# Optimization experiments

Measured on AMD Instinct MI355X. Metric: run time of the kernel, lower is better.

Reference implementation:

```python
import jax, jax.numpy as jnp
import numpy as np

N, C, HW = 32, 256, 64          # batch, in_channels, input_size
K = 128                          # n_clusters
S = 8                            # blocks per side
BLOCK = (HW + S - 1) // S        # = 8, padding_size = 0


def setup_inputs() -> dict:
    key = jax.random.key(0)
    k1, k2 = jax.random.split(key)
    x = jax.random.normal(k1, (N, C, HW, HW), dtype=jnp.float32)
    cluster_centers = jax.random.normal(k2, (K, C), dtype=jnp.float32)
    return {"x": x, "cluster_centers": cluster_centers}


def reference(x, cluster_centers):
    # --- Codebook: argmin over squared distances, computed without the
    x2 = jnp.sum(x * x, axis=1)                       # (N, H, W)
    c2 = jnp.sum(cluster_centers * cluster_centers, axis=1)  # (K,)
    xc = jnp.einsum('nchw,kc->nkhw', x, cluster_centers)     # (N, K, H, W)
    dist = x2[:, None] - 2.0 * xc + c2[None, :, None, None]
    code = jnp.argmin(dist, axis=1)                   # (N, H, W) int

    # --- BlockWiseHistogramEncoder: unfold into S*S non-overlapping
    # BLOCKxBLOCK blocks (padding_size == 0 here), one_hot(code+1), mean ---
    shifted = code + 1                                # values in [1, K]
    n = shifted.shape[0]
    blocks = shifted.reshape(n, S, BLOCK, S, BLOCK)
    blocks = blocks.transpose(0, 1, 3, 2, 4).reshape(n, S * S, BLOCK * BLOCK)
    onehot = (blocks[..., None] == jnp.arange(K + 1)).astype(jnp.float32)
    return onehot.mean(axis=2)                        # (N, S*S, K+1)
```

## Files before the change

### kernel.cpp

```cpp
#include <hip/hip_runtime.h>

#define C_DIM 256
#define K_DIM 128
#define HW_DIM 64
#define PIX 4096
#define N_IMG 32

using short8 = __attribute__((ext_vector_type(8))) short;
using f32x4  = __attribute__((ext_vector_type(4))) float;

__device__ __forceinline__ void lds_barrier() {
    asm volatile("s_waitcnt lgkmcnt(0)\n\ts_barrier" ::: "memory");
}

__device__ __forceinline__ unsigned long long umin64(unsigned long long a, unsigned long long b) {
    return a < b ? a : b;
}
__device__ __forceinline__ unsigned mono(float d) {
    unsigned u = __float_as_uint(d);
    return u ^ ((u & 0x80000000u) ? 0xFFFFFFFFu : 0x80000000u);
}

__device__ __forceinline__ void split3t(float v, unsigned& hu, unsigned& mu, unsigned& lu) {
    unsigned u = __float_as_uint(v);
    unsigned hf = u & 0xffff0000u;
    float r1 = v - __uint_as_float(hf);
    unsigned r1u = __float_as_uint(r1);
    unsigned mf = r1u & 0xffff0000u;
    float r2 = r1 - __uint_as_float(mf);
    hu = u; mu = r1u; lu = __float_as_uint(r2);
}

__global__ __launch_bounds__(64) void prep_kernel(const float* __restrict__ cl,
                                                  unsigned short* __restrict__ Bt,
                                                  float* __restrict__ c2) {
    int k = blockIdx.x;
    int lane = threadIdx.x;
    const float4* row = (const float4*)(cl + k * C_DIM);
    float4 v = row[lane];
    float vv[4] = {v.x, v.y, v.z, v.w};
    unsigned short* bk = Bt + k * 768 + lane * 4;
#pragma unroll
    for (int i = 0; i < 4; ++i) {
        unsigned hu, mu, lu;
        split3t(vv[i], hu, mu, lu);
        bk[i]       = (unsigned short)(hu >> 16);
        bk[256 + i] = (unsigned short)(mu >> 16);
        bk[512 + i] = (unsigned short)(lu >> 16);
    }
    if (lane == 0) {
        float s = 0.f;
#pragma unroll
        for (int i = 0; i < C_DIM / 4; ++i) {
            float4 u = row[i];
            s = fmaf(u.x, u.x, s);
            s = fmaf(u.y, u.y, s);
            s = fmaf(u.z, u.z, s);
            s = fmaf(u.w, u.w, s);
        }
        c2[k] = s;
    }
}

__global__ __launch_bounds__(256) void main_kernel(
    const float* __restrict__ x, const unsigned short* __restrict__ Bt,
    const float* __restrict__ c2v, unsigned char* __restrict__ code) {

    __shared__ __align__(16) unsigned short Ap[3 * 4096];
    __shared__ float x2p[2][128];
    unsigned long long* red = (unsigned long long*)Ap;

    const int t    = threadIdx.x;
    const int lane = t & 63;
    const int w    = t >> 6;
    const int q    = lane >> 4;
    const int l15  = lane & 15;

    const int px = t & 127;
    const int h  = t >> 7;

    const int b   = blockIdx.x;
    const int img = b >> 5;
    const int pb  = (b & 31) * 128;

    const float* xg = x + (size_t)img * (C_DIM * PIX) + pb + px;

    f32x4 acc[8][2];
#pragma unroll
    for (int m = 0; m < 8; ++m)
#pragma unroll
        for (int ns = 0; ns < 2; ++ns) acc[m][ns] = (f32x4){0.f, 0.f, 0.f, 0.f};

    float xr[16];
#pragma unroll
    for (int j = 0; j < 16; ++j) xr[j] = xg[(size_t)(h * 16 + j) * PIX];

    float x2part = 0.f;
    const unsigned short* btb = Bt + (w * 32 + l15) * 768 + q * 8;

    const int wbase = (px >> 4) * 512 + (px & 15) * 8 + h * 2 * 128;

#pragma unroll 1
    for (int ci = 0; ci < 8; ++ci) {
        short8 bv[3][2];
#pragma unroll
        for (int p = 0; p < 3; ++p) {
            bv[p][0] = *(const short8*)(btb + p * 256 + ci * 32);
            bv[p][1] = *(const short8*)(btb + 16 * 768 + p * 256 + ci * 32);
        }

#pragma unroll
        for (int g = 0; g < 2; ++g) {
            unsigned p0[4], p1[4], p2[4];
#pragma unroll
            for (int jj = 0; jj < 4; ++jj) {
                float v0 = xr[g * 8 + jj * 2], v1 = xr[g * 8 + jj * 2 + 1];
                unsigned h0, m0, l0, h1, m1, l1;
                split3t(v0, h0, m0, l0);
                split3t(v1, h1, m1, l1);
                p0[jj] = (h0 >> 16) | (h1 & 0xffff0000u);
                p1[jj] = (m0 >> 16) | (m1 & 0xffff0000u);
                p2[jj] = (l0 >> 16) | (l1 & 0xffff0000u);
                x2part = fmaf(v0, v0, x2part);
                x2part = fmaf(v1, v1, x2part);
            }
            int base = wbase + g * 128;
            *(uint4*)&Ap[base]            = make_uint4(p0[0], p0[1], p0[2], p0[3]);
            *(uint4*)&Ap[4096 + base]     = make_uint4(p1[0], p1[1], p1[2], p1[3]);
            *(uint4*)&Ap[8192 + base]     = make_uint4(p2[0], p2[1], p2[2], p2[3]);
        }
        if (ci == 7) x2p[h][px] = x2part;

        if (ci < 7) {
#pragma unroll
            for (int j = 0; j < 16; ++j)
                xr[j] = xg[(size_t)((ci + 1) * 32 + h * 16 + j) * PIX];
        }

        lds_barrier();

#pragma unroll
        for (int pa = 0; pa < 3; ++pa) {
#pragma unroll
            for (int mg = 0; mg < 4; ++mg) {
                const int m0 = mg * 2, m1 = mg * 2 + 1;
                short8 af0 = *(const short8*)&Ap[pa * 4096 + m0 * 512 + lane * 8];
                short8 af1 = *(const short8*)&Ap[pa * 4096 + m1 * 512 + lane * 8];
#pragma unroll
                for (int pb2 = 0; pb2 < 3; ++pb2) {
                    if (pb2 < 3 - pa) {
                        acc[m0][0] = __builtin_amdgcn_mfma_f32_16x16x32_bf16(af0, bv[pb2][0], acc[m0][0], 0, 0, 0);
                        acc[m0][1] = __builtin_amdgcn_mfma_f32_16x16x32_bf16(af0, bv[pb2][1], acc[m0][1], 0, 0, 0);
                        acc[m1][0] = __builtin_amdgcn_mfma_f32_16x16x32_bf16(af1, bv[pb2][0], acc[m1][0], 0, 0, 0);
                        acc[m1][1] = __builtin_amdgcn_mfma_f32_16x16x32_bf16(af1, bv[pb2][1], acc[m1][1], 0, 0, 0);
                    }
                }
            }
        }
        lds_barrier();
    }

    const float c2a0 = c2v[w * 32 + l15];
    const float c2a1 = c2v[w * 32 + 16 + l15];
    const unsigned n0 = (unsigned)(w * 32 + l15);
    const unsigned n1 = n0 + 16;

#pragma unroll
    for (int m = 0; m < 8; ++m) {
#pragma unroll
        for (int r = 0; r < 4; ++r) {
            int pxl = m * 16 + q * 4 + r;
            float x2v = x2p[0][pxl] + x2p[1][pxl];
            float d0 = (x2v - 2.0f * acc[m][0][r]) + c2a0;
            float d1 = (x2v - 2.0f * acc[m][1][r]) + c2a1;
            unsigned long long k0 = ((unsigned long long)mono(d0) << 32) | n0;
            unsigned long long k1 = ((unsigned long long)mono(d1) << 32) | n1;
            unsigned long long best = umin64(k0, k1);
            best = umin64(best, __shfl_xor(best, 1));
            best = umin64(best, __shfl_xor(best, 2));
            best = umin64(best, __shfl_xor(best, 4));
            best = umin64(best, __shfl_xor(best, 8));
            if (l15 == 0) red[w * 128 + pxl] = best;
        }
    }
    lds_barrier();

    if (t < 128) {
        unsigned long long m0 = umin64(umin64(red[t], red[128 + t]),
                                       umin64(red[256 + t], red[384 + t]));
        code[(size_t)img * PIX + pb + t] = (unsigned char)(m0 & 0xFFu);
    }
}

__global__ __launch_bounds__(256) void hist_kernel(const unsigned char* __restrict__ code,
                                                   float* __restrict__ out) {
    __shared__ int hist[4][K_DIM + 1];
    int wid = threadIdx.x >> 6, lane = threadIdx.x & 63;
    int b = blockIdx.x * 4 + wid;
    int n = b >> 6, sy = (b >> 3) & 7, sx = b & 7;

    hist[wid][lane] = 0;
    hist[wid][lane + 64] = 0;
    if (lane == 0) hist[wid][128] = 0;
    __syncthreads();

    int hh = sy * 8 + (lane >> 3);
    int ww = sx * 8 + (lane & 7);
    int c = code[n * PIX + hh * HW_DIM + ww];
    atomicAdd(&hist[wid][c + 1], 1);
    __syncthreads();

    const float inv = 1.0f / 64.0f;
    out[(size_t)b * (K_DIM + 1) + lane] = hist[wid][lane] * inv;
    out[(size_t)b * (K_DIM + 1) + 64 + lane] = hist[wid][lane + 64] * inv;
    if (lane == 0) out[(size_t)b * (K_DIM + 1) + 128] = hist[wid][128] * inv;
}

extern "C" void kernel_launch(void* const* d_in, const int* in_sizes, int n_in,
                              void* d_out, int out_size, void* d_ws, size_t ws_size,
                              hipStream_t stream) {
    const float* x  = (const float*)d_in[0];
    const float* cl = (const float*)d_in[1];
    float* out = (float*)d_out;

    unsigned short* Bt = (unsigned short*)d_ws;
    float* c2 = (float*)((char*)d_ws + 196608);
    unsigned char* code = (unsigned char*)d_ws + 197120;

    prep_kernel<<<K_DIM, 64, 0, stream>>>(cl, Bt, c2);
    main_kernel<<<(N_IMG * PIX) / 128, 256, 0, stream>>>(x, Bt, c2, code);
    hist_kernel<<<(N_IMG * 64) / 4, 256, 0, stream>>>(code, out);
}
```

Before: 226.3 us.

## Fuse histogram into main kernel and build MFMA operands in registers without LDS

Each block now handles one 64-pixel image row, and the four waves split the work two ways by pixel half and two ways by cluster half. The x operand fragments are split into bf16 pieces directly in registers instead of being staged through LDS, which removes the per-iteration barriers. The histogram kernel and the code buffer are gone: the main kernel adds 1/64 straight into the output with float atomics after a memset. In exchange each wave reloads more B fragments from global memory, and contention on the output atomics may add cost.

```diff
diff --git a/kernel.cpp b/kernel.cpp
--- a/kernel.cpp
+++ b/kernel.cpp
@@ -9,10 +9,6 @@
 using short8 = __attribute__((ext_vector_type(8))) short;
 using f32x4  = __attribute__((ext_vector_type(4))) float;
 
-__device__ __forceinline__ void lds_barrier() {
-    asm volatile("s_waitcnt lgkmcnt(0)\n\ts_barrier" ::: "memory");
-}
-
 __device__ __forceinline__ unsigned long long umin64(unsigned long long a, unsigned long long b) {
     return a < b ? a : b;
 }
@@ -23,11 +19,9 @@
 
 __device__ __forceinline__ void split3t(float v, unsigned& hu, unsigned& mu, unsigned& lu) {
     unsigned u = __float_as_uint(v);
-    unsigned hf = u & 0xffff0000u;
-    float r1 = v - __uint_as_float(hf);
+    float r1 = v - __uint_as_float(u & 0xffff0000u);
     unsigned r1u = __float_as_uint(r1);
-    unsigned mf = r1u & 0xffff0000u;
-    float r2 = r1 - __uint_as_float(mf);
+    float r2 = r1 - __uint_as_float(r1u & 0xffff0000u);
     hu = u; mu = r1u; lu = __float_as_uint(r2);
 }
 
@@ -62,158 +56,156 @@
     }
 }
 
-__global__ __launch_bounds__(256) void main_kernel(
+__global__ __launch_bounds__(256, 4) void main_kernel(
     const float* __restrict__ x, const unsigned short* __restrict__ Bt,
-    const float* __restrict__ c2v, unsigned char* __restrict__ code) {
-
-    __shared__ __align__(16) unsigned short Ap[3 * 4096];
-    __shared__ float x2p[2][128];
-    unsigned long long* red = (unsigned long long*)Ap;
+    const float* __restrict__ c2v, float* __restrict__ out) {
+
+    __shared__ unsigned long long red[2][64];
 
     const int t    = threadIdx.x;
     const int lane = t & 63;
     const int w    = t >> 6;
+    const int pg   = w >> 1;
+    const int kj   = w & 1;
     const int q    = lane >> 4;
     const int l15  = lane & 15;
 
-    const int px = t & 127;
-    const int h  = t >> 7;
-
     const int b   = blockIdx.x;
-    const int img = b >> 5;
-    const int pb  = (b & 31) * 128;
-
-    const float* xg = x + (size_t)img * (C_DIM * PIX) + pb + px;
-
-    f32x4 acc[8][2];
-#pragma unroll
-    for (int m = 0; m < 8; ++m)
-#pragma unroll
-        for (int ns = 0; ns < 2; ++ns) acc[m][ns] = (f32x4){0.f, 0.f, 0.f, 0.f};
-
-    float xr[16];
-#pragma unroll
-    for (int j = 0; j < 16; ++j) xr[j] = xg[(size_t)(h * 16 + j) * PIX];
-
-    float x2part = 0.f;
-    const unsigned short* btb = Bt + (w * 32 + l15) * 768 + q * 8;
-
-    const int wbase = (px >> 4) * 512 + (px & 15) * 8 + h * 2 * 128;
+    const int img = b >> 6;
+    const int row = b & 63;
+
+    const float* xg = x + (size_t)img * (C_DIM * PIX) + row * HW_DIM + pg * 32 + l15;
+
+    const unsigned short* bq0 = Bt + (size_t)(kj * 64 +  0 + l15) * 768 + q * 8;
+    const unsigned short* bq1 = Bt + (size_t)(kj * 64 + 16 + l15) * 768 + q * 8;
+    const unsigned short* bq2 = Bt + (size_t)(kj * 64 + 32 + l15) * 768 + q * 8;
+    const unsigned short* bq3 = Bt + (size_t)(kj * 64 + 48 + l15) * 768 + q * 8;
+
+    f32x4 acc[2][4];
+#pragma unroll
+    for (int mt = 0; mt < 2; ++mt)
+#pragma unroll
+        for (int nt = 0; nt < 4; ++nt) acc[mt][nt] = (f32x4){0.f, 0.f, 0.f, 0.f};
+
+    float x2m[2] = {0.f, 0.f};
+
+    float xv[2][8];
+#pragma unroll
+    for (int mt = 0; mt < 2; ++mt)
+#pragma unroll
+        for (int j = 0; j < 8; ++j)
+            xv[mt][j] = xg[(size_t)(q * 8 + j) * PIX + mt * 16];
 
 #pragma unroll 1
     for (int ci = 0; ci < 8; ++ci) {
-        short8 bv[3][2];
-#pragma unroll
-        for (int p = 0; p < 3; ++p) {
-            bv[p][0] = *(const short8*)(btb + p * 256 + ci * 32);
-            bv[p][1] = *(const short8*)(btb + 16 * 768 + p * 256 + ci * 32);
-        }
-
-#pragma unroll
-        for (int g = 0; g < 2; ++g) {
-            unsigned p0[4], p1[4], p2[4];
+        union U { unsigned u[4]; short8 s; };
+        short8 af[3][2];
+#pragma unroll
+        for (int mt = 0; mt < 2; ++mt) {
+            U ah, am, al;
 #pragma unroll
             for (int jj = 0; jj < 4; ++jj) {
-                float v0 = xr[g * 8 + jj * 2], v1 = xr[g * 8 + jj * 2 + 1];
+                float v0 = xv[mt][2 * jj], v1 = xv[mt][2 * jj + 1];
                 unsigned h0, m0, l0, h1, m1, l1;
                 split3t(v0, h0, m0, l0);
                 split3t(v1, h1, m1, l1);
-                p0[jj] = (h0 >> 16) | (h1 & 0xffff0000u);
-                p1[jj] = (m0 >> 16) | (m1 & 0xffff0000u);
-                p2[jj] = (l0 >> 16) | (l1 & 0xffff0000u);
-                x2part = fmaf(v0, v0, x2part);
-                x2part = fmaf(v1, v1, x2part);
-            }
-            int base = wbase + g * 128;
-            *(uint4*)&Ap[base]            = make_uint4(p0[0], p0[1], p0[2], p0[3]);
-            *(uint4*)&Ap[4096 + base]     = make_uint4(p1[0], p1[1], p1[2], p1[3]);
-            *(uint4*)&Ap[8192 + base]     = make_uint4(p2[0], p2[1], p2[2], p2[3]);
-        }
-        if (ci == 7) x2p[h][px] = x2part;
+                ah.u[jj] = (h0 >> 16) | (h1 & 0xffff0000u);
+                am.u[jj] = (m0 >> 16) | (m1 & 0xffff0000u);
+                al.u[jj] = (l0 >> 16) | (l1 & 0xffff0000u);
+                x2m[mt] = fmaf(v0, v0, x2m[mt]);
+                x2m[mt] = fmaf(v1, v1, x2m[mt]);
+            }
+            af[0][mt] = ah.s; af[1][mt] = am.s; af[2][mt] = al.s;
+        }
 
         if (ci < 7) {
 #pragma unroll
-            for (int j = 0; j < 16; ++j)
-                xr[j] = xg[(size_t)((ci + 1) * 32 + h * 16 + j) * PIX];
-        }
-
-        lds_barrier();
-
-#pragma unroll
-        for (int pa = 0; pa < 3; ++pa) {
-#pragma unroll
-            for (int mg = 0; mg < 4; ++mg) {
-                const int m0 = mg * 2, m1 = mg * 2 + 1;
-                short8 af0 = *(const short8*)&Ap[pa * 4096 + m0 * 512 + lane * 8];
-                short8 af1 = *(const short8*)&Ap[pa * 4096 + m1 * 512 + lane * 8];
-#pragma unroll
-                for (int pb2 = 0; pb2 < 3; ++pb2) {
-                    if (pb2 < 3 - pa) {
-                        acc[m0][0] = __builtin_amdgcn_mfma_f32_16x16x32_bf16(af0, bv[pb2][0], acc[m0][0], 0, 0, 0);
-                        acc[m0][1] = __builtin_amdgcn_mfma_f32_16x16x32_bf16(af0, bv[pb2][1], acc[m0][1], 0, 0, 0);
-                        acc[m1][0] = __builtin_amdgcn_mfma_f32_16x16x32_bf16(af1, bv[pb2][0], acc[m1][0], 0, 0, 0);
-                        acc[m1][1] = __builtin_amdgcn_mfma_f32_16x16x32_bf16(af1, bv[pb2][1], acc[m1][1], 0, 0, 0);
-                    }
-                }
-            }
-        }
-        lds_barrier();
-    }
-
-    const float c2a0 = c2v[w * 32 + l15];
-    const float c2a1 = c2v[w * 32 + 16 + l15];
-    const unsigned n0 = (unsigned)(w * 32 + l15);
-    const unsigned n1 = n0 + 16;
-
-#pragma unroll
-    for (int m = 0; m < 8; ++m) {
+            for (int mt = 0; mt < 2; ++mt)
+#pragma unroll
+                for (int j = 0; j < 8; ++j)
+                    xv[mt][j] = xg[(size_t)((ci + 1) * 32 + q * 8 + j) * PIX + mt * 16];
+        }
+
+        {
+            short8 bf[3][2];
+#pragma unroll
+            for (int p = 0; p < 3; ++p) {
+                bf[p][0] = *(const short8*)(bq0 + p * 256 + ci * 32);
+                bf[p][1] = *(const short8*)(bq1 + p * 256 + ci * 32);
+            }
+#pragma unroll
+            for (int pa = 0; pa < 3; ++pa)
+#pragma unroll
+                for (int mt = 0; mt < 2; ++mt)
+#pragma unroll
+                    for (int ntl = 0; ntl < 2; ++ntl)
+#pragma unroll
+                        for (int pb2 = 0; pb2 < 3; ++pb2)
+                            if (pb2 < 3 - pa)
+                                acc[mt][ntl] = __builtin_amdgcn_mfma_f32_16x16x32_bf16(
+                                    af[pa][mt], bf[pb2][ntl], acc[mt][ntl], 0, 0, 0);
+        }
+        {
+            short8 bf[3][2];
+#pragma unroll
+            for (int p = 0; p < 3; ++p) {
+                bf[p][0] = *(const short8*)(bq2 + p * 256 + ci * 32);
+                bf[p][1] = *(const short8*)(bq3 + p * 256 + ci * 32);
+            }
+#pragma unroll
+            for (int pa = 0; pa < 3; ++pa)
+#pragma unroll
+                for (int mt = 0; mt < 2; ++mt)
+#pragma unroll
+                    for (int ntl = 0; ntl < 2; ++ntl)
+#pragma unroll
+                        for (int pb2 = 0; pb2 < 3; ++pb2)
+                            if (pb2 < 3 - pa)
+                                acc[mt][2 + ntl] = __builtin_amdgcn_mfma_f32_16x16x32_bf16(
+                                    af[pa][mt], bf[pb2][ntl], acc[mt][2 + ntl], 0, 0, 0);
+        }
+    }
+
+#pragma unroll
+    for (int mt = 0; mt < 2; ++mt) {
+        float s = x2m[mt];
+        s += __shfl_xor(s, 16);
+        s += __shfl_xor(s, 32);
+        x2m[mt] = s;
+    }
+
+    float c2l[4];
+#pragma unroll
+    for (int nt = 0; nt < 4; ++nt) c2l[nt] = c2v[kj * 64 + nt * 16 + l15];
+
+#pragma unroll
+    for (int mt = 0; mt < 2; ++mt) {
 #pragma unroll
         for (int r = 0; r < 4; ++r) {
-            int pxl = m * 16 + q * 4 + r;
-            float x2v = x2p[0][pxl] + x2p[1][pxl];
-            float d0 = (x2v - 2.0f * acc[m][0][r]) + c2a0;
-            float d1 = (x2v - 2.0f * acc[m][1][r]) + c2a1;
-            unsigned long long k0 = ((unsigned long long)mono(d0) << 32) | n0;
-            unsigned long long k1 = ((unsigned long long)mono(d1) << 32) | n1;
-            unsigned long long best = umin64(k0, k1);
+            float x2v = __shfl(x2m[mt], q * 4 + r);
+            unsigned long long best = ~0ull;
+#pragma unroll
+            for (int nt = 0; nt < 4; ++nt) {
+                float d = (x2v - 2.0f * acc[mt][nt][r]) + c2l[nt];
+                unsigned long long key = ((unsigned long long)mono(d) << 32)
+                                       | (unsigned)(kj * 64 + nt * 16 + l15);
+                best = umin64(best, key);
+            }
             best = umin64(best, __shfl_xor(best, 1));
             best = umin64(best, __shfl_xor(best, 2));
             best = umin64(best, __shfl_xor(best, 4));
             best = umin64(best, __shfl_xor(best, 8));
-            if (l15 == 0) red[w * 128 + pxl] = best;
-        }
-    }
-    lds_barrier();
-
-    if (t < 128) {
-        unsigned long long m0 = umin64(umin64(red[t], red[128 + t]),
-                                       umin64(red[256 + t], red[384 + t]));
-        code[(size_t)img * PIX + pb + t] = (unsigned char)(m0 & 0xFFu);
-    }
-}
-
-__global__ __launch_bounds__(256) void hist_kernel(const unsigned char* __restrict__ code,
-                                                   float* __restrict__ out) {
-    __shared__ int hist[4][K_DIM + 1];
-    int wid = threadIdx.x >> 6, lane = threadIdx.x & 63;
-    int b = blockIdx.x * 4 + wid;
-    int n = b >> 6, sy = (b >> 3) & 7, sx = b & 7;
-
-    hist[wid][lane] = 0;
-    hist[wid][lane + 64] = 0;
-    if (lane == 0) hist[wid][128] = 0;
+            if (l15 == 0) red[kj][pg * 32 + mt * 16 + q * 4 + r] = best;
+        }
+    }
     __syncthreads();
 
-    int hh = sy * 8 + (lane >> 3);
-    int ww = sx * 8 + (lane & 7);
-    int c = code[n * PIX + hh * HW_DIM + ww];
-    atomicAdd(&hist[wid][c + 1], 1);
-    __syncthreads();
-
-    const float inv = 1.0f / 64.0f;
-    out[(size_t)b * (K_DIM + 1) + lane] = hist[wid][lane] * inv;
-    out[(size_t)b * (K_DIM + 1) + 64 + lane] = hist[wid][lane + 64] * inv;
-    if (lane == 0) out[(size_t)b * (K_DIM + 1) + 128] = hist[wid][128] * inv;
+    if (t < 64) {
+        unsigned long long mk = umin64(red[0][t], red[1][t]);
+        int cl = (int)(mk & 0xFFu);
+        int tile = (row >> 3) * 8 + (t >> 3);
+        atomicAdd(out + ((size_t)img * 64 + tile) * (K_DIM + 1) + cl + 1, 0.015625f);
+    }
 }
 
 extern "C" void kernel_launch(void* const* d_in, const int* in_sizes, int n_in,
@@ -225,9 +217,8 @@
 
     unsigned short* Bt = (unsigned short*)d_ws;
     float* c2 = (float*)((char*)d_ws + 196608);
-    unsigned char* code = (unsigned char*)d_ws + 197120;
-
+
+    hipMemsetAsync(out, 0, (size_t)out_size * sizeof(float), stream);
     prep_kernel<<<K_DIM, 64, 0, stream>>>(cl, Bt, c2);
-    main_kernel<<<(N_IMG * PIX) / 128, 256, 0, stream>>>(x, Bt, c2, code);
-    hist_kernel<<<(N_IMG * 64) / 4, 256, 0, stream>>>(code, out);
-}
+    main_kernel<<<(N_IMG * PIX) / 64, 256, 0, stream>>>(x, Bt, c2, out);
+}
```

New measurement: 270.6 us. 19.5% more time.
